# Kernel tuning notes

Hardware: AMD Instinct MI355X
Metric: run time of the kernel (lower is better)

## Reference

```python
import jax, jax.numpy as jnp
import numpy as np

N_NODES = 120000
EM = 128
N_EDGES = 1920000
BS = 1024
L = 10

def setup_inputs() -> dict:
    key = jax.random.key(0)
    ks = jax.random.split(key, 24)
    stdv = 1.0 / np.sqrt(EM)
    u = lambda k, shape: jax.random.uniform(k, shape, jnp.float32, -stdv, stdv)
    return {
        'src': jax.random.randint(ks[0], (N_EDGES,), 0, N_NODES, jnp.int32),
        'dst': jax.random.randint(ks[1], (N_EDGES,), 0, N_NODES, jnp.int32),
        'user': jax.random.randint(ks[2], (BS, 1), 0, 20000, jnp.int32),
        'seq': jax.random.randint(ks[3], (BS, L), 0, 100000, jnp.int32),
        'mask': jnp.ones((BS, L), jnp.float32),
        'seq_len': jax.random.randint(ks[4], (BS,), 1, L, jnp.int32),
        'pos_idx': jax.random.randint(ks[5], (BS, L), 0, 200, jnp.int32),
        'item_num': 100000,
        'v2e': u(ks[6], (N_NODES, EM)),
        'W_self': u(ks[7], (EM, EM)),
        'W_neigh': u(ks[8], (EM, EM)),
        'sage_b': u(ks[9], (EM,)),
        'pos_emb': u(ks[10], (200, EM)),
        'w1': u(ks[11], (2 * EM, EM)),
        'w2': u(ks[12], (EM, 1)),
        'glu1_w': u(ks[13], (EM, EM)),
        'glu1_b': u(ks[14], (EM,)),
        'glu2_w': u(ks[15], (EM, EM)),
        'w3': u(ks[16], (EM, EM)),
        'w4': u(ks[17], (EM, 1)),
        'glu3_w': u(ks[18], (EM, EM)),
        'glu3_b': u(ks[19], (EM,)),
        'glu4_w': u(ks[20], (EM, EM)),
        'sc_w': u(ks[21], (2 * EM, 1)),
        'sc_b': u(ks[22], (1,)),
    }


def reference(src, dst, user, seq, mask, seq_len, pos_idx, item_num,
              v2e, W_self, W_neigh, sage_b, pos_emb,
              w1, w2, glu1_w, glu1_b, glu2_w,
              w3, w4, glu3_w, glu3_b, glu4_w, sc_w, sc_b):
    N = v2e.shape[0]
    # SAGEConv 'mean': fc_self(x) + fc_neigh(mean over in-neighbors) + bias, then ReLU
    deg = jax.ops.segment_sum(jnp.ones_like(dst, jnp.float32), dst, num_segments=N)
    agg = jax.ops.segment_sum(v2e[src], dst, num_segments=N)
    agg = agg / jnp.clip(deg, 1.0)[:, None]
    h1 = jax.nn.relu(v2e @ W_self + agg @ W_neigh + sage_b)

    u_idx = user + item_num                      # [bs,1]
    node_embeds = (h1[seq] + v2e[seq]) * 0.5     # [bs,L,em]
    user_embeds = (h1[u_idx] + v2e[u_idx]) * 0.5 # [bs,1,em]
    seq_embeds = user_embeds[:, 0]               # [bs,em]

    m = mask[..., None]                          # [bs,L,1]
    # compute_hidden_vector (GLU-gated attention with positional embedding)
    pe = pos_emb[pos_idx]                        # [bs,L,em]
    tmp = jnp.sum(node_embeds * m, axis=1) / jnp.sum(m, axis=1)  # masked mean [bs,em]
    hs = tmp[:, None, :]
    nh = jnp.tanh(jnp.concatenate([pe, node_embeds], -1) @ w1)
    nh = jax.nn.sigmoid(nh @ glu1_w + glu1_b + hs @ glu2_w)
    beta = (nh @ w2) * m
    sess_vec = jnp.sum(beta * node_embeds, axis=1)  # [bs,em]

    # sess_user_vector
    nh2 = jnp.tanh(node_embeds @ w3)
    nh2 = jax.nn.sigmoid(nh2 @ glu3_w + glu3_b + user_embeds @ glu4_w)
    beta2 = (nh2 @ w4) * m
    sess_user = jnp.sum(beta2 * node_embeds, axis=1)  # [bs,em]

    alpha = jax.nn.sigmoid(jnp.concatenate([sess_vec, sess_user], 1) @ sc_w + sc_b)  # [bs,1]
    seq_embeds = seq_embeds + alpha * sess_vec + (1.0 - alpha) * sess_user

    scores = seq_embeds @ v2e[1:].T              # [bs, N-1]
    return scores
```

## Files before the change

kernel.cpp:

```cpp
#include <hip/hip_runtime.h>
#include <stdint.h>

#define N_NODES   120000
#define EM        128
#define N_EDGES_C 1920000
#define BSZ       1024
#define SL        10
#define N_GATHER  (BSZ*SL + BSZ)
#define N_OUTCOL  (N_NODES - 1)
#define NBLK_E    1875
#define CHUNK_E   1024
#define NPANEL    938
#define NBLK_S    (NPANEL*8)

typedef __attribute__((ext_vector_type(8))) short bf16x8;
typedef __attribute__((ext_vector_type(4))) float f32x4;

#define GLOBAL_AS __attribute__((address_space(1)))
#define LDS_AS    __attribute__((address_space(3)))

__device__ inline void gload_lds16(const void* g, void* l) {
  __builtin_amdgcn_global_load_lds((const GLOBAL_AS unsigned int*)g,
                                   (LDS_AS unsigned int*)l, 16, 0, 0);
}

__device__ inline unsigned pk_bf16(float a, float b) {
  unsigned ua = __builtin_bit_cast(unsigned, a);
  ua += 0x7fffu + ((ua >> 16) & 1u);
  unsigned ub = __builtin_bit_cast(unsigned, b);
  ub += 0x7fffu + ((ub >> 16) & 1u);
  return (ua >> 16) | (ub & 0xffff0000u);
}

#define MAP_OFF   0u
#define CNT_OFF   480000u
#define DEG_OFF   480256u
#define OFFS_OFF  525312u
#define CUR_OFF   570368u
#define AGG_OFF   615424u
#define EPAIR_OFF 6382592u
#define SORT_OFF  21742592u
#define BCNT_OFF  (SORT_OFF + 6291456u)
#define BOFF_OFF  (BCNT_OFF + 8192u)
#define NE_OFF    29422592u
#define UE_OFF    34665472u
#define SB_OFF    35189760u
#define V2EB_OFF  37748736u

__global__ __launch_bounds__(256) void k_tobf16(const float* __restrict__ v2e,
    unsigned short* __restrict__ v2eb) {
  size_t base = ((size_t)blockIdx.x*256 + threadIdx.x) * 8;
  float4 v0 = *(const float4*)(v2e + base);
  float4 v1 = *(const float4*)(v2e + base + 4);
  uint4 o;
  o.x = pk_bf16(v0.x, v0.y); o.y = pk_bf16(v0.z, v0.w);
  o.z = pk_bf16(v1.x, v1.y); o.w = pk_bf16(v1.z, v1.w);
  *(uint4*)(v2eb + base) = o;
}

__global__ __launch_bounds__(256) void k_assign(const int* __restrict__ seq,
    const int* __restrict__ user, const int* __restrict__ item_num,
    int* __restrict__ map, int* __restrict__ slotCount) {
  int t = blockIdx.x*256 + threadIdx.x;
  int idx = (t < BSZ*SL) ? seq[t] : (user[t - BSZ*SL] + item_num[0]);
  int old = atomicCAS(map + idx, -1, -2);
  if (old == -1) {
    int slot = atomicAdd(slotCount, 1);
    atomicExch(map + idx, slot);
  }
}

__global__ __launch_bounds__(256) void k_count(const int* __restrict__ src,
    const int* __restrict__ dst, const int* __restrict__ map,
    int* __restrict__ blockCnt, int* __restrict__ deg_i) {
  __shared__ int wsum[4];
  int tid = threadIdx.x, lane = tid & 63, wv = tid >> 6;
  int beg = blockIdx.x * CHUNK_E;
  int local = 0;
  #pragma unroll
  for (int it = 0; it < CHUNK_E/256; ++it) {
    int e = beg + it*256 + tid;
    int slot = map[dst[e]];
    bool flag = slot >= 0;
    if (flag) atomicAdd(deg_i + slot, 1);
    unsigned long long m = __ballot(flag);
    if (lane == 0) local += __popcll(m);
  }
  if (lane == 0) wsum[wv] = local;
  __syncthreads();
  if (tid == 0) blockCnt[blockIdx.x] = wsum[0] + wsum[1] + wsum[2] + wsum[3];
}

__global__ __launch_bounds__(256) void k_scanblk(const int* __restrict__ blockCnt,
    int* __restrict__ blockOffs, int* __restrict__ ecount) {
  __shared__ int wsum[4];
  int tid = threadIdx.x, lane = tid & 63, wv = tid >> 6;
  int carry = 0;
  for (int c = 0; c < 8; ++c) {
    int i = c*256 + tid;
    int v = (i < NBLK_E) ? blockCnt[i] : 0;
    int s = v;
    #pragma unroll
    for (int o = 1; o < 64; o <<= 1) {
      int t = __shfl_up(s, o);
      if (lane >= o) s += t;
    }
    if (lane == 63) wsum[wv] = s;
    __syncthreads();
    int wbase = 0, tot = 0;
    #pragma unroll
    for (int q = 0; q < 4; ++q) { int vq = wsum[q]; if (q < wv) wbase += vq; tot += vq; }
    if (i < NBLK_E) blockOffs[i] = s - v + wbase + carry;
    carry += tot;
    __syncthreads();
  }
  if (tid == 0) ecount[0] = carry;
}

__global__ __launch_bounds__(256) void k_place(const int* __restrict__ src,
    const int* __restrict__ dst, const int* __restrict__ map,
    const int* __restrict__ blockOffs, int* __restrict__ epairs) {
  __shared__ int wsum[4];
  int tid = threadIdx.x, lane = tid & 63, wv = tid >> 6;
  int beg = blockIdx.x * CHUNK_E;
  int base = blockOffs[blockIdx.x];
  int carry = 0;
  #pragma unroll
  for (int it = 0; it < CHUNK_E/256; ++it) {
    int e = beg + it*256 + tid;
    int s = src[e];
    int slot = map[dst[e]];
    bool flag = slot >= 0;
    unsigned long long m = __ballot(flag);
    if (lane == 0) wsum[wv] = __popcll(m);
    __syncthreads();
    int wbase = 0, tot = 0;
    #pragma unroll
    for (int q = 0; q < 4; ++q) { int vq = wsum[q]; if (q < wv) wbase += vq; tot += vq; }
    if (flag) {
      int pos = base + carry + wbase + __popcll(m & ((1ull << lane) - 1ull));
      epairs[2*pos]   = s;
      epairs[2*pos+1] = slot;
    }
    carry += tot;
    __syncthreads();
  }
}

__global__ __launch_bounds__(256) void k_scan(const int* __restrict__ deg_i,
    int* __restrict__ offs, int* __restrict__ cursor) {
  __shared__ int wsum[4];
  int tid = threadIdx.x;
  int lane = tid & 63, wv = tid >> 6;
  int carry = 0;
  for (int c = 0; c < N_GATHER/256; ++c) {
    int i = c*256 + tid;
    int v = deg_i[i];
    int s = v;
    #pragma unroll
    for (int o = 1; o < 64; o <<= 1) {
      int t = __shfl_up(s, o);
      if (lane >= o) s += t;
    }
    if (lane == 63) wsum[wv] = s;
    __syncthreads();
    int wbase = 0;
    #pragma unroll
    for (int q = 0; q < 4; ++q) if (q < wv) wbase += wsum[q];
    int tot = wsum[0] + wsum[1] + wsum[2] + wsum[3];
    int excl = s - v + wbase + carry;
    offs[i] = excl;
    cursor[i] = excl;
    carry += tot;
    __syncthreads();
  }
}

__global__ __launch_bounds__(256) void k_scatter(const int* __restrict__ epairs,
    const int* __restrict__ ecount, int* __restrict__ cursor, int* __restrict__ sorted) {
  int E = ecount[0];
  int T = gridDim.x*blockDim.x;
  for (int e = blockIdx.x*blockDim.x + threadIdx.x; e < E; e += T) {
    int s = epairs[2*e], slot = epairs[2*e+1];
    int pos = atomicAdd(cursor + slot, 1);
    sorted[pos] = s;
  }
}

__global__ __launch_bounds__(256) void k_reduce(const float* __restrict__ v2e,
    const int* __restrict__ offs, const int* __restrict__ deg_i,
    const int* __restrict__ slotCount, const int* __restrict__ sorted,
    float* __restrict__ agg) {
  int nslots = slotCount[0];
  int g = (blockIdx.x*blockDim.x + threadIdx.x) >> 5;
  int lg = threadIdx.x & 31;
  int ngrp = (gridDim.x*blockDim.x) >> 5;
  for (int slot = g; slot < nslots; slot += ngrp) {
    int beg = offs[slot];
    int end = beg + deg_i[slot];
    float4 a = make_float4(0.f, 0.f, 0.f, 0.f);
    for (int e = beg; e < end; ++e) {
      int s = sorted[e];
      const float4 v = *(const float4*)(v2e + (size_t)s*EM + lg*4);
      a.x += v.x; a.y += v.y; a.z += v.z; a.w += v.w;
    }
    *(float4*)(agg + (size_t)slot*EM + lg*4) = a;
  }
}

__global__ __launch_bounds__(128) void k_embed(const int* __restrict__ seq,
    const int* __restrict__ user, const int* __restrict__ item_num,
    const int* __restrict__ map, const int* __restrict__ deg_i,
    const float* __restrict__ agg, const float* __restrict__ v2e,
    const float* __restrict__ W_self, const float* __restrict__ W_neigh,
    const float* __restrict__ sage_b,
    float* __restrict__ node_emb, float* __restrict__ user_emb) {
  __shared__ float xs[8][EM];
  __shared__ float xa[8][EM];
  int j = threadIdx.x;
  int base = blockIdx.x * 8;
  #pragma unroll
  for (int r = 0; r < 8; ++r) {
    int rg = base + r;
    int idx = (rg < BSZ*SL) ? seq[rg] : (user[rg - BSZ*SL] + item_num[0]);
    int slot = map[idx];
    float rd = 1.0f / fmaxf((float)deg_i[slot], 1.0f);
    xs[r][j] = v2e[(size_t)idx*EM + j];
    xa[r][j] = agg[(size_t)slot*EM + j] * rd;
  }
  __syncthreads();
  float acc[8] = {0.f,0.f,0.f,0.f,0.f,0.f,0.f,0.f};
  for (int k = 0; k < EM; ++k) {
    float a  = W_self[k*EM + j];
    float bb = W_neigh[k*EM + j];
    #pragma unroll
    for (int r = 0; r < 8; ++r) acc[r] += xs[r][k]*a + xa[r][k]*bb;
  }
  float bias = sage_b[j];
  #pragma unroll
  for (int r = 0; r < 8; ++r) {
    int rg = base + r;
    float h = fmaxf(acc[r] + bias, 0.0f);
    float emb = 0.5f * (h + xs[r][j]);
    if (rg < BSZ*SL) node_emb[(size_t)rg*EM + j] = emb;
    else             user_emb[(size_t)(rg - BSZ*SL)*EM + j] = emb;
  }
}

__global__ __launch_bounds__(128) void k_session(
    const float* __restrict__ node_emb, const float* __restrict__ user_emb,
    const int* __restrict__ pos_idx, const float* __restrict__ mask_in,
    const float* __restrict__ pos_emb,
    const float* __restrict__ w1, const float* __restrict__ w2,
    const float* __restrict__ glu1_w, const float* __restrict__ glu1_b,
    const float* __restrict__ glu2_w,
    const float* __restrict__ w3, const float* __restrict__ w4,
    const float* __restrict__ glu3_w, const float* __restrict__ glu3_b,
    const float* __restrict__ glu4_w,
    const float* __restrict__ sc_w, const float* __restrict__ sc_b,
    unsigned short* __restrict__ seqb) {
  __shared__ float ne[SL][EM], pe[SL][EM], r1[SL][EM], r2[SL][EM];
  __shared__ float ue[EM], hsS[EM], redA[EM];
  __shared__ float mls[SL], bl1[SL], bl2[SL];
  __shared__ float alphaS;
  int b = blockIdx.x, j = threadIdx.x;
  ue[j] = user_emb[b*EM + j];
  if (j < SL) mls[j] = mask_in[b*SL + j];
  #pragma unroll
  for (int l = 0; l < SL; ++l) {
    ne[l][j] = node_emb[(size_t)(b*SL + l)*EM + j];
    int p = pos_idx[b*SL + l];
    pe[l][j] = pos_emb[(size_t)p*EM + j];
  }
  __syncthreads();
  float s = 0.f, ms = 0.f;
  #pragma unroll
  for (int l = 0; l < SL; ++l) { s += mls[l]*ne[l][j]; ms += mls[l]; }
  hsS[j] = s / ms;
  float a1[SL], a2[SL];
  #pragma unroll
  for (int l = 0; l < SL; ++l) { a1[l] = 0.f; a2[l] = 0.f; }
  for (int k = 0; k < EM; ++k) {
    float wt  = w1[k*EM + j];
    float wb  = w1[(k+EM)*EM + j];
    float w3v = w3[k*EM + j];
    #pragma unroll
    for (int l = 0; l < SL; ++l) {
      a1[l] += pe[l][k]*wt + ne[l][k]*wb;
      a2[l] += ne[l][k]*w3v;
    }
  }
  #pragma unroll
  for (int l = 0; l < SL; ++l) { r1[l][j] = tanhf(a1[l]); r2[l][j] = tanhf(a2[l]); }
  __syncthreads();
  float g1[SL], g2[SL];
  #pragma unroll
  for (int l = 0; l < SL; ++l) { g1[l] = 0.f; g2[l] = 0.f; }
  float hsa = 0.f, uea = 0.f;
  for (int k = 0; k < EM; ++k) {
    float c1 = glu1_w[k*EM + j];
    float c2 = glu2_w[k*EM + j];
    float c3 = glu3_w[k*EM + j];
    float c4 = glu4_w[k*EM + j];
    hsa += hsS[k]*c2;
    uea += ue[k]*c4;
    #pragma unroll
    for (int l = 0; l < SL; ++l) {
      g1[l] += r1[l][k]*c1;
      g2[l] += r2[l][k]*c3;
    }
  }
  float b1 = glu1_b[j], b3 = glu3_b[j];
  float w2v = w2[j], w4v = w4[j];
  __syncthreads();
  #pragma unroll
  for (int l = 0; l < SL; ++l) {
    float s1 = 1.f/(1.f + expf(-(g1[l] + b1 + hsa)));
    float s2 = 1.f/(1.f + expf(-(g2[l] + b3 + uea)));
    r1[l][j] = s1 * w2v;
    r2[l][j] = s2 * w4v;
  }
  __syncthreads();
  if (j < SL) {
    float t1 = 0.f, t2 = 0.f;
    for (int t = 0; t < EM; ++t) { t1 += r1[j][t]; t2 += r2[j][t]; }
    bl1[j] = t1 * mls[j];
    bl2[j] = t2 * mls[j];
  }
  __syncthreads();
  float sv = 0.f, su = 0.f;
  #pragma unroll
  for (int l = 0; l < SL; ++l) { sv += bl1[l]*ne[l][j]; su += bl2[l]*ne[l][j]; }
  redA[j] = sv*sc_w[j] + su*sc_w[EM + j];
  __syncthreads();
  if (j == 0) {
    float t = 0.f;
    for (int k = 0; k < EM; ++k) t += redA[k];
    alphaS = 1.f/(1.f + expf(-(t + sc_b[0])));
  }
  __syncthreads();
  float al = alphaS;
  float val = ue[j] + al*sv + (1.f - al)*su;
  unsigned uv = __builtin_bit_cast(unsigned, val);
  uv += 0x7fffu + ((uv >> 16) & 1u);
  seqb[b*EM + j] = (unsigned short)(uv >> 16);
}

__global__ __launch_bounds__(256, 4) void k_scores(
    const unsigned short* __restrict__ seqb,
    const unsigned short* __restrict__ v2eb, float* __restrict__ out) {
  __shared__ char Bs[32768];
  int tid = threadIdx.x;
  int bid = blockIdx.x;
  int lid = (bid & 7) * (NBLK_S/8) + (bid >> 3);
  int m0 = (lid & 7) * 128;
  int n0 = (lid >> 3) * 128;
  int w = tid >> 6, lane = tid & 63;
  const char* v2eb_c = (const char*)v2eb;
  #pragma unroll
  for (int i = 0; i < 8; ++i) {
    int chunk = i*4 + w;
    int o = chunk*1024 + lane*16;
    int row = o >> 8;
    int c = o & 255;
    int rowg = n0 + 1 + row;
    if (rowg > N_OUTCOL) rowg = N_OUTCOL;
    const void* src = v2eb_c + (size_t)rowg*256 + (c ^ ((row & 7) << 4));
    gload_lds16(src, Bs + chunk*1024);
  }
  asm volatile("s_waitcnt vmcnt(0)");
  __syncthreads();

  int wm = w >> 1, wn = w & 1;
  int lr = lane & 15, lg = lane >> 4;
  f32x4 acc[4][4];
  #pragma unroll
  for (int mi = 0; mi < 4; ++mi)
    #pragma unroll
    for (int ni = 0; ni < 4; ++ni)
      acc[mi][ni] = 0.f;
  #pragma unroll
  for (int ks = 0; ks < 4; ++ks) {
    bf16x8 a[4], bfr[4];
    #pragma unroll
    for (int mi = 0; mi < 4; ++mi)
      a[mi] = *(const bf16x8*)(seqb + (size_t)(m0 + wm*64 + mi*16 + lr)*EM + ks*32 + lg*8);
    #pragma unroll
    for (int ni = 0; ni < 4; ++ni) {
      int row = wn*64 + ni*16 + lr;
      int off = (row*256 + ks*64 + lg*16) ^ ((row & 7) << 4);
      bfr[ni] = *(const bf16x8*)(Bs + off);
    }
    #pragma unroll
    for (int mi = 0; mi < 4; ++mi)
      #pragma unroll
      for (int ni = 0; ni < 4; ++ni)
        acc[mi][ni] = __builtin_amdgcn_mfma_f32_16x16x32_bf16(a[mi], bfr[ni], acc[mi][ni], 0, 0, 0);
  }
  #pragma unroll
  for (int mi = 0; mi < 4; ++mi) {
    #pragma unroll
    for (int ni = 0; ni < 4; ++ni) {
      int col = n0 + wn*64 + ni*16 + lr;
      if (col < N_OUTCOL) {
        size_t base = (size_t)(m0 + wm*64 + mi*16 + lg*4) * N_OUTCOL + col;
        out[base]                       = acc[mi][ni][0];
        out[base + (size_t)N_OUTCOL]    = acc[mi][ni][1];
        out[base + (size_t)2*N_OUTCOL]  = acc[mi][ni][2];
        out[base + (size_t)3*N_OUTCOL]  = acc[mi][ni][3];
      }
    }
  }
}

extern "C" void kernel_launch(void* const* d_in, const int* in_sizes, int n_in,
                              void* d_out, int out_size, void* d_ws, size_t ws_size,
                              hipStream_t stream) {
  const int*   src      = (const int*)d_in[0];
  const int*   dst      = (const int*)d_in[1];
  const int*   user     = (const int*)d_in[2];
  const int*   seq      = (const int*)d_in[3];
  const float* mask     = (const float*)d_in[4];
  const int*   pos_idx  = (const int*)d_in[6];
  const int*   item_num = (const int*)d_in[7];
  const float* v2e      = (const float*)d_in[8];
  const float* W_self   = (const float*)d_in[9];
  const float* W_neigh  = (const float*)d_in[10];
  const float* sage_b   = (const float*)d_in[11];
  const float* pos_emb  = (const float*)d_in[12];
  const float* w1       = (const float*)d_in[13];
  const float* w2       = (const float*)d_in[14];
  const float* glu1_w   = (const float*)d_in[15];
  const float* glu1_b   = (const float*)d_in[16];
  const float* glu2_w   = (const float*)d_in[17];
  const float* w3       = (const float*)d_in[18];
  const float* w4       = (const float*)d_in[19];
  const float* glu3_w   = (const float*)d_in[20];
  const float* glu3_b   = (const float*)d_in[21];
  const float* glu4_w   = (const float*)d_in[22];
  const float* sc_w     = (const float*)d_in[23];
  const float* sc_b     = (const float*)d_in[24];
  float* out = (float*)d_out;
  char*  ws  = (char*)d_ws;

  int*   map       = (int*)(ws + MAP_OFF);
  int*   slotCount = (int*)(ws + CNT_OFF);
  int*   ecount    = slotCount + 1;
  int*   deg_i     = (int*)(ws + DEG_OFF);
  int*   offs      = (int*)(ws + OFFS_OFF);
  int*   cursor    = (int*)(ws + CUR_OFF);
  float* agg       = (float*)(ws + AGG_OFF);
  int*   epairs    = (int*)(ws + EPAIR_OFF);
  int*   sorted    = (int*)(ws + SORT_OFF);
  int*   blockCnt  = (int*)(ws + BCNT_OFF);
  int*   blockOffs = (int*)(ws + BOFF_OFF);
  float* node_emb  = (float*)(ws + NE_OFF);
  float* user_emb  = (float*)(ws + UE_OFF);
  unsigned short* seqb  = (unsigned short*)(ws + SB_OFF);
  unsigned short* v2eb  = (unsigned short*)(ws + V2EB_OFF);

  hipMemsetAsync(map, 0xFF, 480000, stream);
  hipMemsetAsync(ws + CNT_OFF, 0, (DEG_OFF - CNT_OFF) + 45056, stream);
  k_tobf16<<<7500, 256, 0, stream>>>(v2e, v2eb);
  k_assign<<<N_GATHER/256, 256, 0, stream>>>(seq, user, item_num, map, slotCount);
  k_count<<<NBLK_E, 256, 0, stream>>>(src, dst, map, blockCnt, deg_i);
  k_scanblk<<<1, 256, 0, stream>>>(blockCnt, blockOffs, ecount);
  k_place<<<NBLK_E, 256, 0, stream>>>(src, dst, map, blockOffs, epairs);
  k_scan<<<1, 256, 0, stream>>>(deg_i, offs, cursor);
  k_scatter<<<1024, 256, 0, stream>>>(epairs, ecount, cursor, sorted);
  k_reduce<<<1408, 256, 0, stream>>>(v2e, offs, deg_i, slotCount, sorted, agg);
  k_embed<<<N_GATHER/8, 128, 0, stream>>>(seq, user, item_num, map, deg_i, agg, v2e,
                                          W_self, W_neigh, sage_b, node_emb, user_emb);
  k_session<<<BSZ, 128, 0, stream>>>(node_emb, user_emb, pos_idx, mask, pos_emb,
      w1, w2, glu1_w, glu1_b, glu2_w, w3, w4, glu3_w, glu3_b, glu4_w, sc_w, sc_b, seqb);
  k_scores<<<NBLK_S, 256, 0, stream>>>(seqb, v2eb, out);
}
```

Before: 449.7 us.

## Restructure scores GEMM into register-resident A strips streaming B tiles

```diff
diff --git a/kernel.cpp b/kernel.cpp
--- a/kernel.cpp
+++ b/kernel.cpp
@@ -10,19 +10,13 @@
 #define N_OUTCOL  (N_NODES - 1)
 #define NBLK_E    1875
 #define CHUNK_E   1024
-#define NPANEL    938
-#define NBLK_S    (NPANEL*8)
+#define SC_CHUNKS   50
+#define SC_TPC      150
+#define SC_MSTRIPS  32
+#define NBLK_SC     (SC_MSTRIPS * SC_CHUNKS)
 
 typedef __attribute__((ext_vector_type(8))) short bf16x8;
 typedef __attribute__((ext_vector_type(4))) float f32x4;
-
-#define GLOBAL_AS __attribute__((address_space(1)))
-#define LDS_AS    __attribute__((address_space(3)))
-
-__device__ inline void gload_lds16(const void* g, void* l) {
-  __builtin_amdgcn_global_load_lds((const GLOBAL_AS unsigned int*)g,
-                                   (LDS_AS unsigned int*)l, 16, 0, 0);
-}
 
 __device__ inline unsigned pk_bf16(float a, float b) {
   unsigned ua = __builtin_bit_cast(unsigned, a);
@@ -349,65 +343,42 @@
 __global__ __launch_bounds__(256, 4) void k_scores(
     const unsigned short* __restrict__ seqb,
     const unsigned short* __restrict__ v2eb, float* __restrict__ out) {
-  __shared__ char Bs[32768];
-  int tid = threadIdx.x;
   int bid = blockIdx.x;
-  int lid = (bid & 7) * (NBLK_S/8) + (bid >> 3);
-  int m0 = (lid & 7) * 128;
-  int n0 = (lid >> 3) * 128;
-  int w = tid >> 6, lane = tid & 63;
-  const char* v2eb_c = (const char*)v2eb;
-  #pragma unroll
-  for (int i = 0; i < 8; ++i) {
-    int chunk = i*4 + w;
-    int o = chunk*1024 + lane*16;
-    int row = o >> 8;
-    int c = o & 255;
-    int rowg = n0 + 1 + row;
-    if (rowg > N_OUTCOL) rowg = N_OUTCOL;
-    const void* src = v2eb_c + (size_t)rowg*256 + (c ^ ((row & 7) << 4));
-    gload_lds16(src, Bs + chunk*1024);
-  }
-  asm volatile("s_waitcnt vmcnt(0)");
-  __syncthreads();
-
-  int wm = w >> 1, wn = w & 1;
+  int lid = (bid & 7) * (NBLK_SC/8) + (bid >> 3);
+  int chunk = lid >> 5;
+  int ms    = lid & 31;
+  int m0 = ms * 32;
+  int w = threadIdx.x >> 6, lane = threadIdx.x & 63;
   int lr = lane & 15, lg = lane >> 4;
-  f32x4 acc[4][4];
-  #pragma unroll
-  for (int mi = 0; mi < 4; ++mi)
-    #pragma unroll
-    for (int ni = 0; ni < 4; ++ni)
-      acc[mi][ni] = 0.f;
+  bf16x8 a0[4], a1f[4];
   #pragma unroll
   for (int ks = 0; ks < 4; ++ks) {
-    bf16x8 a[4], bfr[4];
-    #pragma unroll
-    for (int mi = 0; mi < 4; ++mi)
-      a[mi] = *(const bf16x8*)(seqb + (size_t)(m0 + wm*64 + mi*16 + lr)*EM + ks*32 + lg*8);
-    #pragma unroll
-    for (int ni = 0; ni < 4; ++ni) {
-      int row = wn*64 + ni*16 + lr;
-      int off = (row*256 + ks*64 + lg*16) ^ ((row & 7) << 4);
-      bfr[ni] = *(const bf16x8*)(Bs + off);
-    }
-    #pragma unroll
-    for (int mi = 0; mi < 4; ++mi)
+    a0[ks]  = *(const bf16x8*)(seqb + (size_t)(m0 + lr)*EM      + ks*32 + lg*8);
+    a1f[ks] = *(const bf16x8*)(seqb + (size_t)(m0 + 16 + lr)*EM + ks*32 + lg*8);
+  }
+  int start = w * 38;
+  int cnt = SC_TPC - start; if (cnt > 38) cnt = 38;
+  int tg0 = chunk * SC_TPC + start;
+  for (int t = 0; t < cnt; ++t) {
+    int n0 = (tg0 + t) * 16;
+    int brow = n0 + lr + 1;
+    if (brow > N_OUTCOL) brow = N_OUTCOL;
+    const unsigned short* bp = v2eb + (size_t)brow*EM;
+    f32x4 acc0 = {0.f,0.f,0.f,0.f}, acc1 = {0.f,0.f,0.f,0.f};
+    #pragma unroll
+    for (int ks = 0; ks < 4; ++ks) {
+      bf16x8 b = *(const bf16x8*)(bp + ks*32 + lg*8);
+      acc0 = __builtin_amdgcn_mfma_f32_16x16x32_bf16(a0[ks],  b, acc0, 0, 0, 0);
+      acc1 = __builtin_amdgcn_mfma_f32_16x16x32_bf16(a1f[ks], b, acc1, 0, 0, 0);
+    }
+    int col = n0 + lr;
+    if (col < N_OUTCOL) {
+      size_t base0 = (size_t)(m0 + lg*4) * N_OUTCOL + col;
+      size_t base1 = (size_t)(m0 + 16 + lg*4) * N_OUTCOL + col;
       #pragma unroll
-      for (int ni = 0; ni < 4; ++ni)
-        acc[mi][ni] = __builtin_amdgcn_mfma_f32_16x16x32_bf16(a[mi], bfr[ni], acc[mi][ni], 0, 0, 0);
-  }
-  #pragma unroll
-  for (int mi = 0; mi < 4; ++mi) {
-    #pragma unroll
-    for (int ni = 0; ni < 4; ++ni) {
-      int col = n0 + wn*64 + ni*16 + lr;
-      if (col < N_OUTCOL) {
-        size_t base = (size_t)(m0 + wm*64 + mi*16 + lg*4) * N_OUTCOL + col;
-        out[base]                       = acc[mi][ni][0];
-        out[base + (size_t)N_OUTCOL]    = acc[mi][ni][1];
-        out[base + (size_t)2*N_OUTCOL]  = acc[mi][ni][2];
-        out[base + (size_t)3*N_OUTCOL]  = acc[mi][ni][3];
+      for (int r = 0; r < 4; ++r) {
+        out[base0 + (size_t)r * N_OUTCOL] = acc0[r];
+        out[base1 + (size_t)r * N_OUTCOL] = acc1[r];
       }
     }
   }
@@ -473,5 +444,5 @@
                                           W_self, W_neigh, sage_b, node_emb, user_emb);
   k_session<<<BSZ, 128, 0, stream>>>(node_emb, user_emb, pos_idx, mask, pos_emb,
       w1, w2, glu1_w, glu1_b, glu2_w, w3, w4, glu3_w, glu3_b, glu4_w, sc_w, sc_b, seqb);
-  k_scores<<<NBLK_S, 256, 0, stream>>>(seqb, v2eb, out);
-}
+  k_scores<<<NBLK_SC, 256, 0, stream>>>(seqb, v2eb, out);
+}
```

Measured after the change: 549.6 us. +22.2%, slower.
